# Kernel optimization log

Measured on AMD Instinct MI355X. Metric: run time of the kernel, lower is better.

Reference implementation:

```python
import jax, jax.numpy as jnp
import numpy as np

B, N, E, H = 4, 2048, 512, 8
D = E // H  # head dim = 64


def setup_inputs() -> dict:
    key = jax.random.key(0)
    ks = jax.random.split(key, 5)
    s = 1.0 / np.sqrt(E)
    return {
        "x": jax.random.normal(ks[0], (B, N, E), dtype=jnp.float32),
        "Wk": jax.random.normal(ks[1], (E, E), dtype=jnp.float32) * s,
        "bk": jax.random.normal(ks[2], (E,), dtype=jnp.float32) * s,
        "Wv": jax.random.normal(ks[3], (E, E), dtype=jnp.float32) * s,
        "bv": jax.random.normal(ks[4], (E,), dtype=jnp.float32) * s,
    }


def reference(x, Wk, bk, Wv, bv):
    b, n, e = x.shape
    # Linear projections (torch Linear: y = x @ W.T + b), split into heads.
    keys = (x @ Wk.T + bk).reshape(b, n, H, D).transpose(0, 2, 1, 3)    # b h n d
    values = (x @ Wv.T + bv).reshape(b, n, H, D).transpose(0, 2, 1, 3)  # b h n d
    # Q = K self-attention: scores [b, h, n, n]
    dotprod = jnp.einsum('bhnd,bhmd->bhnm', keys, keys)
    # softmax over last axis, then unusual POST-softmax scaling by sqrt(emb)
    att = jax.nn.softmax(dotprod, axis=-1) / jnp.sqrt(jnp.asarray(e, x.dtype))
    # dropout p=0 -> identity
    out = jnp.einsum('bhnm,bhmd->bhnd', att, values)
    return out.transpose(0, 2, 1, 3).reshape(b, n, e)
```

## Files before the change

### kernel.cpp

```cpp
#include <hip/hip_runtime.h>

typedef __bf16 bf16_t;
typedef bf16_t bf16x8 __attribute__((ext_vector_type(8)));
typedef float f32x4 __attribute__((ext_vector_type(4)));

#define NSEQ 2048
#define EMB 512
#define HEADS 8
#define HD 64
#define BATCH 4
#define LOG2E 1.4426950408889634f

#define MFMA16(a, b, c) __builtin_amdgcn_mfma_f32_16x16x32_bf16(a, b, c, 0, 0, 0)


__global__ __launch_bounds__(256, 2) void proj_kernel(
    const float* __restrict__ x,
    const float* __restrict__ Wk, const float* __restrict__ bk,
    const float* __restrict__ Wv, const float* __restrict__ bv,
    bf16_t* __restrict__ Kf, bf16_t* __restrict__ Vf)
{
  __shared__ union {
    struct {
      __align__(16) bf16_t A[2][128][40];
      __align__(16) bf16_t B[2][128][40];
    } s;
    __align__(16) bf16_t T[128][136];
  } u;

  const int t    = threadIdx.x;
  const int w    = t >> 6;
  const int lane = t & 63;
  const int quad = lane >> 4;
  const int l15  = lane & 15;
  const int wr   = w >> 1, wc = w & 1;
  const int m0   = blockIdx.x * 128;
  const int n0   = blockIdx.y * 128;
  const int zz   = (blockIdx.y >= 4);
  const float* __restrict__ W = zz ? Wv : Wk;
  const int nW = n0 - zz * 512;

  const int sr = t >> 3;
  const int sj = t & 7;
  const int sb = sj >> 2, sc = (sj & 3) * 8;

  float4 pa[4][2], pb[4][2];
  auto prefetch = [&](int k0) {
#pragma unroll
    for (int i = 0; i < 4; ++i) {
      const float* xa = x + (size_t)(m0 + sr + i * 32) * EMB + k0 + sj * 8;
      const float* wa = W + (size_t)(nW + sr + i * 32) * EMB + k0 + sj * 8;
      pa[i][0] = *(const float4*)xa; pa[i][1] = *(const float4*)(xa + 4);
      pb[i][0] = *(const float4*)wa; pb[i][1] = *(const float4*)(wa + 4);
    }
  };
  auto pack8 = [](float4 a, float4 b) -> bf16x8 {
    bf16x8 v;
    v[0] = (bf16_t)a.x; v[1] = (bf16_t)a.y; v[2] = (bf16_t)a.z; v[3] = (bf16_t)a.w;
    v[4] = (bf16_t)b.x; v[5] = (bf16_t)b.y; v[6] = (bf16_t)b.z; v[7] = (bf16_t)b.w;
    return v;
  };

  f32x4 acc[4][4] = {};
  prefetch(0);

  for (int it = 0; it < 8; ++it) {
    __syncthreads();
#pragma unroll
    for (int i = 0; i < 4; ++i) {
      *(bf16x8*)(&u.s.A[sb][sr + i * 32][sc]) = pack8(pa[i][0], pa[i][1]);
      *(bf16x8*)(&u.s.B[sb][sr + i * 32][sc]) = pack8(pb[i][0], pb[i][1]);
    }
    __syncthreads();
    if (it < 7) prefetch((it + 1) * 64);

    bf16x8 af[4][2], bf[4][2];
#pragma unroll
    for (int mt = 0; mt < 4; ++mt)
#pragma unroll
      for (int kk = 0; kk < 2; ++kk)
        af[mt][kk] = *(const bf16x8*)(&u.s.A[kk][wr * 64 + mt * 16 + l15][quad * 8]);
#pragma unroll
    for (int nt = 0; nt < 4; ++nt)
#pragma unroll
      for (int kk = 0; kk < 2; ++kk)
        bf[nt][kk] = *(const bf16x8*)(&u.s.B[kk][wc * 64 + nt * 16 + l15][quad * 8]);
#pragma unroll
    for (int kk = 0; kk < 2; ++kk)
#pragma unroll
      for (int mt = 0; mt < 4; ++mt)
#pragma unroll
        for (int nt = 0; nt < 4; ++nt)
          acc[mt][nt] = MFMA16(af[mt][kk], bf[nt][kk], acc[mt][nt]);
  }

  __syncthreads();

#pragma unroll
  for (int mt = 0; mt < 4; ++mt) {
#pragma unroll
    for (int nt = 0; nt < 4; ++nt) {
      const int F = wc * 64 + nt * 16 + l15;
      const int c = n0 + F;
      const float bb = zz ? bv[c - 512] : bk[c];
#pragma unroll
      for (int reg = 0; reg < 4; ++reg) {
        const int R = wr * 64 + mt * 16 + quad * 4 + reg;
        const float v = acc[mt][nt][reg] + bb;
        if (!zz) u.T[R][F] = (bf16_t)v;
        else     u.T[F][R] = (bf16_t)v;
      }
    }
  }
  __syncthreads();

  if (!zz) {
#pragma unroll
    for (int i = 0; i < 8; ++i) {
      const int fi  = i * 4 + w;
      const int hL  = fi >> 4, kk = (fi >> 3) & 1, ktl = fi & 7;
      const bf16x8 v = *(const bf16x8*)(&u.T[ktl * 16 + l15][hL * 64 + kk * 32 + quad * 8]);
      const int gr = m0 + ktl * 16 + l15;
      const int b = gr >> 11, n = gr & (NSEQ - 1);
      const int bh = b * HEADS + (n0 >> 6) + hL;
      bf16_t* dst = Kf + (((size_t)(bh * 128 + (n >> 4)) * 2 + kk)) * 512 + lane * 8;
      *(bf16x8*)dst = v;
    }
  } else {
#pragma unroll
    for (int i = 0; i < 8; ++i) {
      const int fi   = i * 4 + w;
      const int hL   = fi >> 4, dt = (fi >> 2) & 3, k32l = fi & 3;
      const bf16_t* Trow = &u.T[hL * 64 + dt * 16 + l15][0];
      const int r0 = k32l * 32 + (quad >> 1) * 16 + (quad & 1) * 4;
      union { uint2 d2[2]; bf16x8 v; } vv;
      vv.d2[0] = *(const uint2*)(Trow + r0);
      vv.d2[1] = *(const uint2*)(Trow + r0 + 8);
      const int gr = m0 + k32l * 32;
      const int b = gr >> 11, n = gr & (NSEQ - 1);
      const int bh = b * HEADS + ((n0 - 512) >> 6) + hL;
      bf16_t* dst = Vf + (((size_t)(bh * 64 + (n >> 5)) * 4 + dt)) * 512 + lane * 8;
      *(bf16x8*)dst = vv.v;
    }
  }
}

__global__ __launch_bounds__(256, 2) void flash_kernel(
    const bf16_t* __restrict__ Kf, const bf16_t* __restrict__ Vf,
    float* __restrict__ out)
{
  __shared__ struct {
    __align__(16) float Cb[2][4096];
    __align__(16) float Lb[2][64][16];
  } u;

  const int t    = threadIdx.x;
  const int w    = t >> 6;
  const int lane = t & 63;
  const int quad = lane >> 4;
  const int l15  = lane & 15;
  const int rh   = w & 1;
  const int kh   = w >> 1;

  const int bh = blockIdx.x;
  const int b  = bh >> 3, h = bh & 7;
  const int rowbase = blockIdx.y * 128 + rh * 64;
  const int qtile   = rowbase >> 4;

  const bf16_t* __restrict__ Kb = Kf + (size_t)bh * 128 * 2 * 512;
  const bf16_t* __restrict__ Vb = Vf + (size_t)bh * 64 * 4 * 512;

  bf16x8 qf[4][2];
#pragma unroll
  for (int nt = 0; nt < 4; ++nt)
#pragma unroll
    for (int kk = 0; kk < 2; ++kk)
      qf[nt][kk] = *(const bf16x8*)(Kb + ((size_t)(qtile + nt) * 2 + kk) * 512 + lane * 8);

  float mlog[4];
#pragma unroll
  for (int nt = 0; nt < 4; ++nt) {
    float ss = 0.f;
#pragma unroll
    for (int kk = 0; kk < 2; ++kk)
#pragma unroll
      for (int j = 0; j < 8; ++j) {
        const float qv = (float)qf[nt][kk][j];
        ss = fmaf(qv, qv, ss);
      }
    ss += __shfl_xor(ss, 16, 64);
    ss += __shfl_xor(ss, 32, 64);
    mlog[nt] = ss * LOG2E;
  }

  bf16x8 ones;
#pragma unroll
  for (int j = 0; j < 8; ++j) ones[j] = (bf16_t)1.0f;

  f32x4 acco[4][4] = {};
  f32x4 accll[4]   = {};

  auto load_k = [&](int kt, bf16x8 (&dst)[2][2]) {
    const int kb = kt * 4 + kh * 2;
#pragma unroll
    for (int jt = 0; jt < 2; ++jt)
#pragma unroll
      for (int kk = 0; kk < 2; ++kk)
        dst[jt][kk] =
            *(const bf16x8*)(Kb + ((size_t)(kb + jt) * 2 + kk) * 512 + lane * 8);
  };

  auto body = [&](int kt, bf16x8 (&kcur)[2][2], bf16x8 (&knxt)[2][2]) {
    bf16x8 vf[4];
    const int v32 = kt * 2 + kh;
#pragma unroll
    for (int dt = 0; dt < 4; ++dt)
      vf[dt] = *(const bf16x8*)(Vb + ((size_t)v32 * 4 + dt) * 512 + lane * 8);

    f32x4 st[2][4] = {};
    __builtin_amdgcn_s_setprio(1);
#pragma unroll
    for (int kk = 0; kk < 2; ++kk)
#pragma unroll
      for (int jt = 0; jt < 2; ++jt)
#pragma unroll
        for (int nt = 0; nt < 4; ++nt)
          st[jt][nt] = MFMA16(kcur[jt][kk], qf[nt][kk], st[jt][nt]);
    __builtin_amdgcn_s_setprio(0);

    load_k(kt + 1 < NSEQ / 64 ? kt + 1 : kt, knxt);

    bf16x8 pf[4];
#pragma unroll
    for (int nt = 0; nt < 4; ++nt) {
      union { bf16_t h[2]; unsigned uu; } w00, w01, w10, w11;
      w00.h[0] = (bf16_t)__builtin_amdgcn_exp2f(fmaf(st[0][nt][0], LOG2E, -mlog[nt]));
      w00.h[1] = (bf16_t)__builtin_amdgcn_exp2f(fmaf(st[0][nt][1], LOG2E, -mlog[nt]));
      w01.h[0] = (bf16_t)__builtin_amdgcn_exp2f(fmaf(st[0][nt][2], LOG2E, -mlog[nt]));
      w01.h[1] = (bf16_t)__builtin_amdgcn_exp2f(fmaf(st[0][nt][3], LOG2E, -mlog[nt]));
      w10.h[0] = (bf16_t)__builtin_amdgcn_exp2f(fmaf(st[1][nt][0], LOG2E, -mlog[nt]));
      w10.h[1] = (bf16_t)__builtin_amdgcn_exp2f(fmaf(st[1][nt][1], LOG2E, -mlog[nt]));
      w11.h[0] = (bf16_t)__builtin_amdgcn_exp2f(fmaf(st[1][nt][2], LOG2E, -mlog[nt]));
      w11.h[1] = (bf16_t)__builtin_amdgcn_exp2f(fmaf(st[1][nt][3], LOG2E, -mlog[nt]));
      auto r0 = __builtin_amdgcn_permlane32_swap(w00.uu, w10.uu, false, false);
      auto r1 = __builtin_amdgcn_permlane32_swap(w01.uu, w11.uu, false, false);
      union { unsigned uw[4]; bf16x8 v; } pk;
      pk.uw[0] = r0[0]; pk.uw[1] = r1[0]; pk.uw[2] = r0[1]; pk.uw[3] = r1[1];
      pf[nt] = pk.v;
    }

    __builtin_amdgcn_s_setprio(1);
#pragma unroll
    for (int rt = 0; rt < 4; ++rt) {
      accll[rt] = MFMA16(pf[rt], ones, accll[rt]);
#pragma unroll
      for (int dt = 0; dt < 4; ++dt)
        acco[rt][dt] = MFMA16(pf[rt], vf[dt], acco[rt][dt]);
    }
    __builtin_amdgcn_s_setprio(0);
  };

  bf16x8 kA[2][2], kB[2][2];
  load_k(0, kA);
  for (int kt = 0; kt < NSEQ / 64; kt += 2) {
    body(kt,     kA, kB);
    body(kt + 1, kB, kA);
  }

  __syncthreads();
  if (kh == 1) {
#pragma unroll
    for (int rt = 0; rt < 4; ++rt) {
#pragma unroll
      for (int dt = 0; dt < 4; ++dt)
        *(f32x4*)(&u.Cb[rh][((rt * 4 + dt) * 64 + lane) * 4]) = acco[rt][dt];
      *(f32x4*)(&u.Lb[rh][lane][rt * 4]) = accll[rt];
    }
  }
  __syncthreads();
  if (kh == 0) {
#pragma unroll
    for (int rt = 0; rt < 4; ++rt) {
#pragma unroll
      for (int dt = 0; dt < 4; ++dt)
        acco[rt][dt] += *(const f32x4*)(&u.Cb[rh][((rt * 4 + dt) * 64 + lane) * 4]);
      accll[rt] += *(const f32x4*)(&u.Lb[rh][lane][rt * 4]);
    }

    const float SCL = 0.044194173824159216f;
#pragma unroll
    for (int rt = 0; rt < 4; ++rt)
#pragma unroll
      for (int reg = 0; reg < 4; ++reg) {
        const float f = SCL / accll[rt][reg];
        const int n = rowbase + rt * 16 + quad * 4 + reg;
#pragma unroll
        for (int dt = 0; dt < 4; ++dt)
          out[((size_t)(b * NSEQ + n)) * EMB + h * HD + dt * 16 + l15] =
              acco[rt][dt][reg] * f;
      }
  }
}

extern "C" void kernel_launch(void* const* d_in, const int* in_sizes, int n_in,
                              void* d_out, int out_size, void* d_ws, size_t ws_size,
                              hipStream_t stream) {
  const float* x  = (const float*)d_in[0];
  const float* Wk = (const float*)d_in[1];
  const float* bk = (const float*)d_in[2];
  const float* Wv = (const float*)d_in[3];
  const float* bv = (const float*)d_in[4];
  float* out = (float*)d_out;

  bf16_t* Kf = (bf16_t*)d_ws;
  bf16_t* Vf = Kf + (size_t)BATCH * HEADS * NSEQ * HD;

  dim3 pg(8192 / 128, 1024 / 128);
  proj_kernel<<<pg, 256, 0, stream>>>(x, Wk, bk, Wv, bv, Kf, Vf);

  dim3 fg(BATCH * HEADS, NSEQ / 128);
  flash_kernel<<<fg, 256, 0, stream>>>(Kf, Vf, out);
}
```

Measured before the change: 129.2 us.

## Software-pipeline QK^T MFMAs one tile ahead and replace ones-MFMA row sum with VALU sums

Restructures the flash loop so the score MFMAs for the next key tile are issued interleaved with the exp2/pack work of the current tile, with K loads prefetched two tiles ahead. The row-sum of probabilities is now accumulated in fp32 registers and reduced with shuffles instead of an extra MFMA against a ones vector, and the s_setprio hints are removed. This aims to overlap matrix and vector work and cut MFMA count, at the cost of more live registers (two score buffers) which may pressure occupancy at launch bounds 256,2. The denominator now sums fp32 exps instead of bf16-rounded values, which slightly changes numerics.

```diff
diff --git a/kernel.cpp b/kernel.cpp
--- a/kernel.cpp
+++ b/kernel.cpp
@@ -151,7 +151,7 @@
 {
   __shared__ struct {
     __align__(16) float Cb[2][4096];
-    __align__(16) float Lb[2][64][16];
+    __align__(16) float Lb[2][2][64];
   } u;
 
   const int t    = threadIdx.x;
@@ -193,12 +193,9 @@
     mlog[nt] = ss * LOG2E;
   }
 
-  bf16x8 ones;
-#pragma unroll
-  for (int j = 0; j < 8; ++j) ones[j] = (bf16_t)1.0f;
-
   f32x4 acco[4][4] = {};
-  f32x4 accll[4]   = {};
+  float lsum[4] = {0.f, 0.f, 0.f, 0.f};
+  const f32x4 fz = {};
 
   auto load_k = [&](int kt, bf16x8 (&dst)[2][2]) {
     const int kb = kt * 4 + kh * 2;
@@ -210,38 +207,40 @@
             *(const bf16x8*)(Kb + ((size_t)(kb + jt) * 2 + kk) * 512 + lane * 8);
   };
 
-  auto body = [&](int kt, bf16x8 (&kcur)[2][2], bf16x8 (&knxt)[2][2]) {
+  auto body = [&](int kt, f32x4 (&stC)[2][4], f32x4 (&stN)[2][4],
+                  bf16x8 (&kN)[2][2], bf16x8 (&kF)[2][2]) {
     bf16x8 vf[4];
     const int v32 = kt * 2 + kh;
 #pragma unroll
     for (int dt = 0; dt < 4; ++dt)
       vf[dt] = *(const bf16x8*)(Vb + ((size_t)v32 * 4 + dt) * 512 + lane * 8);
 
-    f32x4 st[2][4] = {};
-    __builtin_amdgcn_s_setprio(1);
-#pragma unroll
-    for (int kk = 0; kk < 2; ++kk)
-#pragma unroll
-      for (int jt = 0; jt < 2; ++jt)
-#pragma unroll
-        for (int nt = 0; nt < 4; ++nt)
-          st[jt][nt] = MFMA16(kcur[jt][kk], qf[nt][kk], st[jt][nt]);
-    __builtin_amdgcn_s_setprio(0);
-
-    load_k(kt + 1 < NSEQ / 64 ? kt + 1 : kt, knxt);
+    load_k(kt + 2 < NSEQ / 64 ? kt + 2 : NSEQ / 64 - 1, kF);
 
     bf16x8 pf[4];
 #pragma unroll
     for (int nt = 0; nt < 4; ++nt) {
+      stN[0][nt] = MFMA16(kN[0][0], qf[nt][0], fz);
+      stN[1][nt] = MFMA16(kN[1][0], qf[nt][0], fz);
+      stN[0][nt] = MFMA16(kN[0][1], qf[nt][1], stN[0][nt]);
+      stN[1][nt] = MFMA16(kN[1][1], qf[nt][1], stN[1][nt]);
+
+      const float m = mlog[nt];
+      const float e0 = __builtin_amdgcn_exp2f(fmaf(stC[0][nt][0], LOG2E, -m));
+      const float e1 = __builtin_amdgcn_exp2f(fmaf(stC[0][nt][1], LOG2E, -m));
+      const float e2 = __builtin_amdgcn_exp2f(fmaf(stC[0][nt][2], LOG2E, -m));
+      const float e3 = __builtin_amdgcn_exp2f(fmaf(stC[0][nt][3], LOG2E, -m));
+      const float e4 = __builtin_amdgcn_exp2f(fmaf(stC[1][nt][0], LOG2E, -m));
+      const float e5 = __builtin_amdgcn_exp2f(fmaf(stC[1][nt][1], LOG2E, -m));
+      const float e6 = __builtin_amdgcn_exp2f(fmaf(stC[1][nt][2], LOG2E, -m));
+      const float e7 = __builtin_amdgcn_exp2f(fmaf(stC[1][nt][3], LOG2E, -m));
+      lsum[nt] += ((e0 + e1) + (e2 + e3)) + ((e4 + e5) + (e6 + e7));
+
       union { bf16_t h[2]; unsigned uu; } w00, w01, w10, w11;
-      w00.h[0] = (bf16_t)__builtin_amdgcn_exp2f(fmaf(st[0][nt][0], LOG2E, -mlog[nt]));
-      w00.h[1] = (bf16_t)__builtin_amdgcn_exp2f(fmaf(st[0][nt][1], LOG2E, -mlog[nt]));
-      w01.h[0] = (bf16_t)__builtin_amdgcn_exp2f(fmaf(st[0][nt][2], LOG2E, -mlog[nt]));
-      w01.h[1] = (bf16_t)__builtin_amdgcn_exp2f(fmaf(st[0][nt][3], LOG2E, -mlog[nt]));
-      w10.h[0] = (bf16_t)__builtin_amdgcn_exp2f(fmaf(st[1][nt][0], LOG2E, -mlog[nt]));
-      w10.h[1] = (bf16_t)__builtin_amdgcn_exp2f(fmaf(st[1][nt][1], LOG2E, -mlog[nt]));
-      w11.h[0] = (bf16_t)__builtin_amdgcn_exp2f(fmaf(st[1][nt][2], LOG2E, -mlog[nt]));
-      w11.h[1] = (bf16_t)__builtin_amdgcn_exp2f(fmaf(st[1][nt][3], LOG2E, -mlog[nt]));
+      w00.h[0] = (bf16_t)e0; w00.h[1] = (bf16_t)e1;
+      w01.h[0] = (bf16_t)e2; w01.h[1] = (bf16_t)e3;
+      w10.h[0] = (bf16_t)e4; w10.h[1] = (bf16_t)e5;
+      w11.h[0] = (bf16_t)e6; w11.h[1] = (bf16_t)e7;
       auto r0 = __builtin_amdgcn_permlane32_swap(w00.uu, w10.uu, false, false);
       auto r1 = __builtin_amdgcn_permlane32_swap(w01.uu, w11.uu, false, false);
       union { unsigned uw[4]; bf16x8 v; } pk;
@@ -249,51 +248,61 @@
       pf[nt] = pk.v;
     }
 
-    __builtin_amdgcn_s_setprio(1);
-#pragma unroll
-    for (int rt = 0; rt < 4; ++rt) {
-      accll[rt] = MFMA16(pf[rt], ones, accll[rt]);
+#pragma unroll
+    for (int rt = 0; rt < 4; ++rt)
 #pragma unroll
       for (int dt = 0; dt < 4; ++dt)
         acco[rt][dt] = MFMA16(pf[rt], vf[dt], acco[rt][dt]);
-    }
-    __builtin_amdgcn_s_setprio(0);
   };
 
   bf16x8 kA[2][2], kB[2][2];
+  f32x4 stA[2][4], stB[2][4];
   load_k(0, kA);
+  load_k(1, kB);
+#pragma unroll
+  for (int nt = 0; nt < 4; ++nt) {
+    stA[0][nt] = MFMA16(kA[0][0], qf[nt][0], fz);
+    stA[1][nt] = MFMA16(kA[1][0], qf[nt][0], fz);
+    stA[0][nt] = MFMA16(kA[0][1], qf[nt][1], stA[0][nt]);
+    stA[1][nt] = MFMA16(kA[1][1], qf[nt][1], stA[1][nt]);
+  }
+
   for (int kt = 0; kt < NSEQ / 64; kt += 2) {
-    body(kt,     kA, kB);
-    body(kt + 1, kB, kA);
-  }
-
-  __syncthreads();
+    body(kt,     stA, stB, kB, kA);
+    body(kt + 1, stB, stA, kA, kB);
+  }
+
+#pragma unroll
+  for (int nt = 0; nt < 4; ++nt) {
+    lsum[nt] += __shfl_xor(lsum[nt], 16, 64);
+    lsum[nt] += __shfl_xor(lsum[nt], 32, 64);
+    u.Lb[kh][rh][nt * 16 + l15] = lsum[nt];
+  }
+
   if (kh == 1) {
 #pragma unroll
-    for (int rt = 0; rt < 4; ++rt) {
+    for (int rt = 0; rt < 4; ++rt)
 #pragma unroll
       for (int dt = 0; dt < 4; ++dt)
         *(f32x4*)(&u.Cb[rh][((rt * 4 + dt) * 64 + lane) * 4]) = acco[rt][dt];
-      *(f32x4*)(&u.Lb[rh][lane][rt * 4]) = accll[rt];
-    }
   }
   __syncthreads();
   if (kh == 0) {
 #pragma unroll
-    for (int rt = 0; rt < 4; ++rt) {
+    for (int rt = 0; rt < 4; ++rt)
 #pragma unroll
       for (int dt = 0; dt < 4; ++dt)
         acco[rt][dt] += *(const f32x4*)(&u.Cb[rh][((rt * 4 + dt) * 64 + lane) * 4]);
-      accll[rt] += *(const f32x4*)(&u.Lb[rh][lane][rt * 4]);
-    }
 
     const float SCL = 0.044194173824159216f;
 #pragma unroll
     for (int rt = 0; rt < 4; ++rt)
 #pragma unroll
       for (int reg = 0; reg < 4; ++reg) {
-        const float f = SCL / accll[rt][reg];
-        const int n = rowbase + rt * 16 + quad * 4 + reg;
+        const int r = rt * 16 + quad * 4 + reg;
+        const float l = u.Lb[0][rh][r] + u.Lb[1][rh][r];
+        const float f = SCL / l;
+        const int n = rowbase + r;
 #pragma unroll
         for (int dt = 0; dt < 4; ++dt)
           out[((size_t)(b * NSEQ + n)) * EMB + h * HD + dt * 16 + l15] =
```

Result: slower. 142.9 us (+10.6%).

## Pre-convert inputs to bf16 and stage GEMM tiles via direct global-to-LDS loads

Applied to the files above, without the earlier changes.

Adds a separate kernel that converts x, Wk and Wv to bf16 once, using the output buffer as scratch. The projection GEMM then loads bf16 tiles straight into LDS with global_load_lds and an XOR-swizzled layout, replacing the register prefetch, convert and LDS store path. This halves the bytes the GEMM reads and removes conversion work from its inner loop. In exchange it adds a kernel launch and a full extra pass over x, and drops the register prefetch overlap, so each K step now waits on its loads.

```diff
diff --git a/kernel.cpp b/kernel.cpp
--- a/kernel.cpp
+++ b/kernel.cpp
@@ -11,19 +11,47 @@
 #define BATCH 4
 #define LOG2E 1.4426950408889634f
 
+#define XELEMS (BATCH * NSEQ * EMB)
+#define WELEMS (EMB * EMB)
+
 #define MFMA16(a, b, c) __builtin_amdgcn_mfma_f32_16x16x32_bf16(a, b, c, 0, 0, 0)
 
 
+__global__ __launch_bounds__(256) void convert_kernel(
+    const float* __restrict__ x, const float* __restrict__ Wk,
+    const float* __restrict__ Wv, bf16_t* __restrict__ xb)
+{
+  const int i = blockIdx.x * 256 + threadIdx.x;
+  const float* src;
+  size_t off;
+  bf16_t* dst;
+  if (i < XELEMS / 8) {
+    off = (size_t)i * 8;
+    src = x;
+    dst = xb + off;
+  } else {
+    const size_t e = (size_t)(i - XELEMS / 8) * 8;
+    if (e < WELEMS) { src = Wk; off = e; }
+    else            { src = Wv; off = e - WELEMS; }
+    dst = xb + XELEMS + e;
+  }
+  const float4 a = *(const float4*)(src + off);
+  const float4 b = *(const float4*)(src + off + 4);
+  bf16x8 v;
+  v[0] = (bf16_t)a.x; v[1] = (bf16_t)a.y; v[2] = (bf16_t)a.z; v[3] = (bf16_t)a.w;
+  v[4] = (bf16_t)b.x; v[5] = (bf16_t)b.y; v[6] = (bf16_t)b.z; v[7] = (bf16_t)b.w;
+  *(bf16x8*)dst = v;
+}
+
 __global__ __launch_bounds__(256, 2) void proj_kernel(
-    const float* __restrict__ x,
-    const float* __restrict__ Wk, const float* __restrict__ bk,
-    const float* __restrict__ Wv, const float* __restrict__ bv,
+    const bf16_t* __restrict__ xb, const bf16_t* __restrict__ Wb,
+    const float* __restrict__ bk, const float* __restrict__ bv,
     bf16_t* __restrict__ Kf, bf16_t* __restrict__ Vf)
 {
   __shared__ union {
     struct {
-      __align__(16) bf16_t A[2][128][40];
-      __align__(16) bf16_t B[2][128][40];
+      __align__(16) bf16_t A[128 * 64];
+      __align__(16) bf16_t B[128 * 64];
     } s;
     __align__(16) bf16_t T[128][136];
   } u;
@@ -37,64 +65,59 @@
   const int m0   = blockIdx.x * 128;
   const int n0   = blockIdx.y * 128;
   const int zz   = (blockIdx.y >= 4);
-  const float* __restrict__ W = zz ? Wv : Wk;
-  const int nW = n0 - zz * 512;
-
-  const int sr = t >> 3;
-  const int sj = t & 7;
-  const int sb = sj >> 2, sc = (sj & 3) * 8;
-
-  float4 pa[4][2], pb[4][2];
-  auto prefetch = [&](int k0) {
-#pragma unroll
-    for (int i = 0; i < 4; ++i) {
-      const float* xa = x + (size_t)(m0 + sr + i * 32) * EMB + k0 + sj * 8;
-      const float* wa = W + (size_t)(nW + sr + i * 32) * EMB + k0 + sj * 8;
-      pa[i][0] = *(const float4*)xa; pa[i][1] = *(const float4*)(xa + 4);
-      pb[i][0] = *(const float4*)wa; pb[i][1] = *(const float4*)(wa + 4);
-    }
-  };
-  auto pack8 = [](float4 a, float4 b) -> bf16x8 {
-    bf16x8 v;
-    v[0] = (bf16_t)a.x; v[1] = (bf16_t)a.y; v[2] = (bf16_t)a.z; v[3] = (bf16_t)a.w;
-    v[4] = (bf16_t)b.x; v[5] = (bf16_t)b.y; v[6] = (bf16_t)b.z; v[7] = (bf16_t)b.w;
-    return v;
+
+  const int rsub = lane >> 3;
+  const int cswz = (lane & 7) ^ rsub;
+
+  auto stage = [&](int it) {
+    const int kb = it * 64;
+#pragma unroll
+    for (int g = 0; g < 4; ++g) {
+      const int r = w * 32 + g * 8;
+      const bf16_t* gA = xb + (size_t)(m0 + r + rsub) * EMB + kb + cswz * 8;
+      const bf16_t* gB = Wb + (size_t)(n0 + r + rsub) * EMB + kb + cswz * 8;
+      __builtin_amdgcn_global_load_lds(
+          (const __attribute__((address_space(1))) void*)gA,
+          (__attribute__((address_space(3))) void*)&u.s.A[r * 64], 16, 0, 0);
+      __builtin_amdgcn_global_load_lds(
+          (const __attribute__((address_space(1))) void*)gB,
+          (__attribute__((address_space(3))) void*)&u.s.B[r * 64], 16, 0, 0);
+    }
+  };
+  auto rdA = [&](int R, int c) {
+    return *(const bf16x8*)(&u.s.A[R * 64 + ((c ^ (R & 7)) << 3)]);
+  };
+  auto rdB = [&](int R, int c) {
+    return *(const bf16x8*)(&u.s.B[R * 64 + ((c ^ (R & 7)) << 3)]);
   };
 
   f32x4 acc[4][4] = {};
-  prefetch(0);
 
   for (int it = 0; it < 8; ++it) {
+    stage(it);
     __syncthreads();
-#pragma unroll
-    for (int i = 0; i < 4; ++i) {
-      *(bf16x8*)(&u.s.A[sb][sr + i * 32][sc]) = pack8(pa[i][0], pa[i][1]);
-      *(bf16x8*)(&u.s.B[sb][sr + i * 32][sc]) = pack8(pb[i][0], pb[i][1]);
-    }
+
+    bf16x8 af[4][2], bfr[4][2];
+#pragma unroll
+    for (int mt = 0; mt < 4; ++mt)
+#pragma unroll
+      for (int kk = 0; kk < 2; ++kk)
+        af[mt][kk] = rdA(wr * 64 + mt * 16 + l15, kk * 4 + quad);
+#pragma unroll
+    for (int nt = 0; nt < 4; ++nt)
+#pragma unroll
+      for (int kk = 0; kk < 2; ++kk)
+        bfr[nt][kk] = rdB(wc * 64 + nt * 16 + l15, kk * 4 + quad);
+#pragma unroll
+    for (int kk = 0; kk < 2; ++kk)
+#pragma unroll
+      for (int mt = 0; mt < 4; ++mt)
+#pragma unroll
+        for (int nt = 0; nt < 4; ++nt)
+          acc[mt][nt] = MFMA16(af[mt][kk], bfr[nt][kk], acc[mt][nt]);
+
     __syncthreads();
-    if (it < 7) prefetch((it + 1) * 64);
-
-    bf16x8 af[4][2], bf[4][2];
-#pragma unroll
-    for (int mt = 0; mt < 4; ++mt)
-#pragma unroll
-      for (int kk = 0; kk < 2; ++kk)
-        af[mt][kk] = *(const bf16x8*)(&u.s.A[kk][wr * 64 + mt * 16 + l15][quad * 8]);
-#pragma unroll
-    for (int nt = 0; nt < 4; ++nt)
-#pragma unroll
-      for (int kk = 0; kk < 2; ++kk)
-        bf[nt][kk] = *(const bf16x8*)(&u.s.B[kk][wc * 64 + nt * 16 + l15][quad * 8]);
-#pragma unroll
-    for (int kk = 0; kk < 2; ++kk)
-#pragma unroll
-      for (int mt = 0; mt < 4; ++mt)
-#pragma unroll
-        for (int nt = 0; nt < 4; ++nt)
-          acc[mt][nt] = MFMA16(af[mt][kk], bf[nt][kk], acc[mt][nt]);
-  }
-
-  __syncthreads();
+  }
 
 #pragma unroll
   for (int mt = 0; mt < 4; ++mt) {
@@ -315,8 +338,14 @@
   bf16_t* Kf = (bf16_t*)d_ws;
   bf16_t* Vf = Kf + (size_t)BATCH * HEADS * NSEQ * HD;
 
+  bf16_t* xb = (bf16_t*)d_out;
+  bf16_t* Wb = xb + XELEMS;
+
+  convert_kernel<<<(XELEMS / 8 + 2 * WELEMS / 8) / 256, 256, 0, stream>>>(
+      x, Wk, Wv, xb);
+
   dim3 pg(8192 / 128, 1024 / 128);
-  proj_kernel<<<pg, 256, 0, stream>>>(x, Wk, bk, Wv, bv, Kf, Vf);
+  proj_kernel<<<pg, 256, 0, stream>>>(xb, Wb, bk, bv, Kf, Vf);
 
   dim3 fg(BATCH * HEADS, NSEQ / 128);
   flash_kernel<<<fg, 256, 0, stream>>>(Kf, Vf, out);
```

Result: no change. 131.0 us (+1.4%).
